# Kernel optimization log

Measured on AMD Instinct MI355X. Metric: run time of the kernel, lower is better.

The kernel has to match this reference:

```python
import jax, jax.numpy as jnp
import numpy as np

B, T, I, H, D, V = 4, 512, 512, 8, 512, 32000


def setup_inputs() -> dict:
    key = jax.random.key(0)
    ks = jax.random.split(key, 7)
    return {
        "inp_tokens": jax.random.randint(ks[0], (B, I), 0, V, dtype=jnp.int32),
        "tar_embedded": jax.random.normal(ks[1], (B, T, D), dtype=jnp.float32),
        "generator_output": jax.random.uniform(ks[2], (B, T, V), dtype=jnp.float32),
        "enc_output": jax.random.normal(ks[3], (B, I, D), dtype=jnp.float32),
        "dec_state": jax.random.normal(ks[4], (B, T, D), dtype=jnp.float32),
        "attn_heads": jax.random.uniform(ks[5], (B, H, T, I), dtype=jnp.float32),
        "W_pgen": jax.random.normal(ks[6], (3 * D, 1), dtype=jnp.float32) * 0.02,
        "b_pgen": jnp.zeros((1,), dtype=jnp.float32),
    }


def reference(inp_tokens, tar_embedded, generator_output, enc_output, dec_state,
              attn_heads, W_pgen, b_pgen):
    vocab = generator_output.shape[-1]
    # mean over heads: (B,T,I)
    attn = jnp.mean(attn_heads, axis=1)
    # attention-weighted context: (B,T,D)
    context = jnp.einsum('bti,bid->btd', attn, enc_output)
    # p_gen gate: Dense(1) on concat -> sigmoid, shape (B,T,1)
    p_gen_inputs = jnp.concatenate([context, dec_state, tar_embedded], axis=-1)
    p_gen = jax.nn.sigmoid(p_gen_inputs @ W_pgen + b_pgen)
    # pointer distribution: scatter-add attn weights into vocab slots
    # (equivalent to einsum('bti,biv->btv', attn, one_hot(inp_tokens)))
    def scatter_one(a, idx):  # a: (T,I), idx: (I,) -> (T,V)
        return jnp.zeros((a.shape[0], vocab), a.dtype).at[:, idx].add(a)
    pointer_output = jax.vmap(scatter_one)(attn, inp_tokens)
    pointer_output = jax.nn.softmax(pointer_output, axis=-1)
    # gated mixture of generator and pointer distributions: (B,T,V)
    final_output = p_gen * generator_output + (1.0 - p_gen) * pointer_output
    return (final_output, pointer_output, jnp.squeeze(p_gen, axis=-1))
```

## Files before the change

kernel.cpp:

```cpp
#include <hip/hip_runtime.h>
#include <math.h>

#define B 4
#define T 512
#define I 512
#define H 8
#define D 512
#define V 32000

__global__ void k_attn_mean(const float* __restrict__ ah, float* __restrict__ attn) {
    long long idx4 = (long long)blockIdx.x * blockDim.x + threadIdx.x;
    const long long total4 = (long long)B * T * I / 4;
    if (idx4 >= total4) return;
    long long flat = idx4 * 4;
    long long b = flat / ((long long)T * I);
    long long rem = flat - b * (long long)T * I;
    const float4* src = (const float4*)(ah + b * (long long)H * T * I + rem);
    const long long stride4 = (long long)T * I / 4;
    float4 s = src[0];
#pragma unroll
    for (int h = 1; h < H; ++h) {
        float4 x = src[h * stride4];
        s.x += x.x; s.y += x.y; s.z += x.z; s.w += x.w;
    }
    const float r = 1.0f / (float)H;
    s.x *= r; s.y *= r; s.z *= r; s.w *= r;
    ((float4*)attn)[idx4] = s;
}

__global__ void k_leaders(const int* __restrict__ tok, int* __restrict__ leader) {
    __shared__ int t_lds[I];
    const int b = blockIdx.x;
    const int i = threadIdx.x;
    t_lds[i] = tok[b * I + i];
    __syncthreads();
    const int mytok = t_lds[i];
    int lead = i;
    for (int j = 0; j < i; ++j) {
        if (t_lds[j] == mytok) { lead = j; break; }
    }
    leader[b * I + i] = lead;
}

__global__ void k_vb(const float* __restrict__ enc, const float* __restrict__ W,
                     float* __restrict__ vb) {
    const int row = blockIdx.x * 4 + (threadIdx.x >> 6);
    const int lane = threadIdx.x & 63;
    const float* e = enc + (long long)row * D;
    float p = 0.f;
    for (int d = lane; d < D; d += 64) p += e[d] * W[d];
#pragma unroll
    for (int o = 32; o > 0; o >>= 1) p += __shfl_down(p, o, 64);
    if (lane == 0) vb[row] = p;
}

__global__ void k_pgen(const float* __restrict__ attn, const float* __restrict__ vb,
                       const float* __restrict__ dec, const float* __restrict__ tar,
                       const float* __restrict__ W, const float* __restrict__ bptr,
                       float* __restrict__ pgen) {
    const int row = blockIdx.x * 4 + (threadIdx.x >> 6);
    const int lane = threadIdx.x & 63;
    const int b = row / T;
    const float* ar = attn + (long long)row * I;
    const float* vr = vb + b * I;
    const float* dr = dec + (long long)row * D;
    const float* tr = tar + (long long)row * D;
    float p = 0.f;
    for (int k = lane; k < I; k += 64) p += ar[k] * vr[k];
    for (int k = lane; k < D; k += 64) p += dr[k] * W[D + k] + tr[k] * W[2 * D + k];
#pragma unroll
    for (int o = 32; o > 0; o >>= 1) p += __shfl_down(p, o, 64);
    if (lane == 0) {
        const float x = p + bptr[0];
        pgen[row] = 1.0f / (1.0f + __expf(-x));
    }
}

__global__ void __launch_bounds__(256) k_main(
    const float* __restrict__ attn, const int* __restrict__ tok,
    const int* __restrict__ leader, const float* __restrict__ gen,
    const float* __restrict__ pgen, float* __restrict__ final_out,
    float* __restrict__ pointer_out) {
    __shared__ float c[I];
    __shared__ float e[I];
    __shared__ int tk[I];
    __shared__ int ld[I];
    __shared__ float red[4];
    __shared__ float s_inv, s_pg;

    const int row = blockIdx.x;
    const int b = row / T;
    const int tid = threadIdx.x;

    const float* ar = attn + (long long)row * I;
    const int* tb = tok + b * I;
    const int* lb = leader + b * I;

    for (int i = tid; i < I; i += 256) { c[i] = 0.f; tk[i] = tb[i]; ld[i] = lb[i]; }
    __syncthreads();
    for (int i = tid; i < I; i += 256) atomicAdd(&c[ld[i]], ar[i]);
    __syncthreads();

    float local = 0.f;
    for (int i = tid; i < I; i += 256) {
        if (ld[i] == i) {
            const float ei = __expf(c[i]);
            e[i] = ei;
            local += ei - 1.0f;
        }
    }
#pragma unroll
    for (int o = 32; o > 0; o >>= 1) local += __shfl_down(local, o, 64);
    const int lane = tid & 63, w = tid >> 6;
    if (lane == 0) red[w] = local;
    __syncthreads();
    if (tid == 0) {
        const float denom = (float)V + red[0] + red[1] + red[2] + red[3];
        s_inv = 1.0f / denom;
        s_pg = pgen[row];
    }
    __syncthreads();

    const float inv = s_inv, pg = s_pg, omp = 1.0f - pg;
    const size_t base = (size_t)row * V;
    const float4* g4 = (const float4*)(gen + base);
    float4* f4 = (float4*)(final_out + base);
    float4* p4 = (float4*)(pointer_out + base);
    const float fb_add = omp * inv;
    const float4 pconst = make_float4(inv, inv, inv, inv);
    for (int v4 = tid; v4 < V / 4; v4 += 256) {
        const float4 g = g4[v4];
        float4 f;
        f.x = pg * g.x + fb_add; f.y = pg * g.y + fb_add;
        f.z = pg * g.z + fb_add; f.w = pg * g.w + fb_add;
        f4[v4] = f;
        p4[v4] = pconst;
    }
    __syncthreads();
    for (int i = tid; i < I; i += 256) {
        if (ld[i] == i) {
            const int slot = tk[i];
            const float pv = e[i] * inv;
            pointer_out[base + slot] = pv;
            final_out[base + slot] = pg * gen[base + slot] + omp * pv;
        }
    }
}

extern "C" void kernel_launch(void* const* d_in, const int* in_sizes, int n_in,
                              void* d_out, int out_size, void* d_ws, size_t ws_size,
                              hipStream_t stream) {
    const int* inp_tokens = (const int*)d_in[0];
    const float* tar = (const float*)d_in[1];
    const float* gen = (const float*)d_in[2];
    const float* enc = (const float*)d_in[3];
    const float* dec = (const float*)d_in[4];
    const float* ah  = (const float*)d_in[5];
    const float* W   = (const float*)d_in[6];
    const float* b0  = (const float*)d_in[7];

    float* out = (float*)d_out;
    const size_t BTV = (size_t)B * T * V;
    float* final_out   = out;
    float* pointer_out = out + BTV;
    float* pgen_out    = out + 2 * BTV;

    char* ws = (char*)d_ws;
    float* attn  = (float*)ws;
    int* leader  = (int*)(ws + sizeof(float) * (size_t)B * T * I);
    float* vb    = (float*)((char*)leader + sizeof(int) * (size_t)B * I);

    k_attn_mean<<<(B * T * I / 4 + 255) / 256, 256, 0, stream>>>(ah, attn);
    k_leaders<<<B, I, 0, stream>>>(inp_tokens, leader);
    k_vb<<<(B * I) / 4, 256, 0, stream>>>(enc, W, vb);
    k_pgen<<<(B * T) / 4, 256, 0, stream>>>(attn, vb, dec, tar, W, b0, pgen_out);
    k_main<<<B * T, 256, 0, stream>>>(attn, inp_tokens, leader, gen, pgen_out,
                                      final_out, pointer_out);
}
```

Baseline: 867.1 us.

## Fuse sparse pointer scatter into dense vocab write via shared bitmap and hash

Builds a shared-memory bitmap of occupied vocab slots and a hash table mapping token to exp value, so the dense streaming loop writes the final values of pointer and final outputs in a single pass. This removes the second scattered-write phase, the extra barrier, and the redundant overwrite of up to 512 slots per row. The cost is about 12KB more LDS per block, atomics during setup, and divergent hash probes inside the streaming loop.

```diff
diff --git a/kernel.cpp b/kernel.cpp
--- a/kernel.cpp
+++ b/kernel.cpp
@@ -7,6 +7,8 @@
 #define H 8
 #define D 512
 #define V 32000
+#define HASH_SZ 1024
+#define BM_WORDS (V / 32)
 
 __global__ void k_attn_mean(const float* __restrict__ ah, float* __restrict__ attn) {
     long long idx4 = (long long)blockIdx.x * blockDim.x + threadIdx.x;
@@ -76,15 +78,26 @@
     }
 }
 
+__device__ __forceinline__ float hash_probe(const int* hkey, const float* hval, int slot) {
+    int h = slot & (HASH_SZ - 1);
+    while (true) {
+        const int k = hkey[h];
+        if (k == slot) return hval[h];
+        h = (h + 1) & (HASH_SZ - 1);
+    }
+}
+
 __global__ void __launch_bounds__(256) k_main(
     const float* __restrict__ attn, const int* __restrict__ tok,
     const int* __restrict__ leader, const float* __restrict__ gen,
     const float* __restrict__ pgen, float* __restrict__ final_out,
     float* __restrict__ pointer_out) {
     __shared__ float c[I];
-    __shared__ float e[I];
     __shared__ int tk[I];
     __shared__ int ld[I];
+    __shared__ unsigned bm[BM_WORDS];
+    __shared__ int hkey[HASH_SZ];
+    __shared__ float hval[HASH_SZ];
     __shared__ float red[4];
     __shared__ float s_inv, s_pg;
 
@@ -97,6 +110,8 @@
     const int* lb = leader + b * I;
 
     for (int i = tid; i < I; i += 256) { c[i] = 0.f; tk[i] = tb[i]; ld[i] = lb[i]; }
+    for (int i = tid; i < BM_WORDS; i += 256) bm[i] = 0u;
+    for (int i = tid; i < HASH_SZ; i += 256) hkey[i] = -1;
     __syncthreads();
     for (int i = tid; i < I; i += 256) atomicAdd(&c[ld[i]], ar[i]);
     __syncthreads();
@@ -104,9 +119,13 @@
     float local = 0.f;
     for (int i = tid; i < I; i += 256) {
         if (ld[i] == i) {
+            const int slot = tk[i];
             const float ei = __expf(c[i]);
-            e[i] = ei;
             local += ei - 1.0f;
+            atomicOr(&bm[slot >> 5], 1u << (slot & 31));
+            int h = slot & (HASH_SZ - 1);
+            while (atomicCAS(&hkey[h], -1, slot) != -1) h = (h + 1) & (HASH_SZ - 1);
+            hval[h] = ei;
         }
     }
 #pragma unroll
@@ -126,24 +145,24 @@
     const float4* g4 = (const float4*)(gen + base);
     float4* f4 = (float4*)(final_out + base);
     float4* p4 = (float4*)(pointer_out + base);
-    const float fb_add = omp * inv;
-    const float4 pconst = make_float4(inv, inv, inv, inv);
     for (int v4 = tid; v4 < V / 4; v4 += 256) {
         const float4 g = g4[v4];
+        const unsigned nib = (bm[v4 >> 3] >> ((v4 & 7) << 2)) & 0xFu;
+        float4 p = make_float4(inv, inv, inv, inv);
+        if (nib) {
+            const int s0 = v4 << 2;
+            if (nib & 1u) p.x = hash_probe(hkey, hval, s0) * inv;
+            if (nib & 2u) p.y = hash_probe(hkey, hval, s0 + 1) * inv;
+            if (nib & 4u) p.z = hash_probe(hkey, hval, s0 + 2) * inv;
+            if (nib & 8u) p.w = hash_probe(hkey, hval, s0 + 3) * inv;
+        }
         float4 f;
-        f.x = pg * g.x + fb_add; f.y = pg * g.y + fb_add;
-        f.z = pg * g.z + fb_add; f.w = pg * g.w + fb_add;
+        f.x = fmaf(pg, g.x, omp * p.x);
+        f.y = fmaf(pg, g.y, omp * p.y);
+        f.z = fmaf(pg, g.z, omp * p.z);
+        f.w = fmaf(pg, g.w, omp * p.w);
         f4[v4] = f;
-        p4[v4] = pconst;
-    }
-    __syncthreads();
-    for (int i = tid; i < I; i += 256) {
-        if (ld[i] == i) {
-            const int slot = tk[i];
-            const float pv = e[i] * inv;
-            pointer_out[base + slot] = pv;
-            final_out[base + slot] = pg * gen[base + slot] + omp * pv;
-        }
+        p4[v4] = p;
     }
 }
 
```

After: 792.9 us. -8.6%, faster.
